# Optimization experiments

Measured on AMD Instinct MI355X. Metric: run time of the kernel, lower is better.

The kernel has to match this reference:

```python
import jax, jax.numpy as jnp
import numpy as np

B, Cin, Cout, H, W, K, S, P = 8, 128, 128, 64, 64, 3, 1, 1


def setup_inputs() -> dict:
    key = jax.random.key(0)
    k1, k2, k3 = jax.random.split(key, 3)
    x = jax.random.normal(k1, (B, Cin, H, W), jnp.float32)
    # offset-predicting conv weight (zero-init in the original; use small random for a nontrivial test)
    w_offset = jax.random.normal(k2, (2 * K * K, Cin, K, K), jnp.float32) * 0.01
    # deformable conv weight, uniform(-stdv, stdv) with stdv = 1/sqrt(Cin*K*K)
    stdv = 1.0 / np.sqrt(Cin * K * K)
    w = jax.random.uniform(k3, (Cout, Cin, K, K), jnp.float32, -stdv, stdv)
    return {"x": x, "w_offset": w_offset, "w": w}


def _conv2d(x, w, stride, pad):
    return jax.lax.conv_general_dilated(
        x, w, (stride, stride), [(pad, pad), (pad, pad)],
        dimension_numbers=("NCHW", "OIHW", "NCHW"))


def _deform_conv(x, offset, w, stride, pad):
    # x: [B,C,H,W]; offset: [B,2*K*K,Ho,Wo] as (dy,dx) pairs per kernel tap; w: [Cout,C,K,K]
    Bb, C, Hh, Ww = x.shape
    Co, _, Kk, _ = w.shape
    _, _, Ho, Wo = offset.shape
    KK = Kk * Kk
    off = offset.reshape(Bb, KK, 2, Ho, Wo)
    dy, dx = off[:, :, 0], off[:, :, 1]              # [B,KK,Ho,Wo]

    ky, kx = jnp.meshgrid(jnp.arange(Kk), jnp.arange(Kk), indexing="ij")
    ky = ky.reshape(KK).astype(x.dtype)
    kx = kx.reshape(KK).astype(x.dtype)
    oy = (jnp.arange(Ho) * stride - pad).astype(x.dtype)
    ox = (jnp.arange(Wo) * stride - pad).astype(x.dtype)

    # absolute sampling coordinates per kernel tap: [B,KK,Ho,Wo]
    py = oy[None, None, :, None] + ky[None, :, None, None] + dy
    px = ox[None, None, None, :] + kx[None, :, None, None] + dx

    y0 = jnp.floor(py)
    x0 = jnp.floor(px)
    ly = py - y0
    lx = px - x0
    y0i = y0.astype(jnp.int32)
    x0i = x0.astype(jnp.int32)

    xf = x.reshape(Bb, C, Hh * Ww)

    def gather(yi, xi):
        valid = (yi >= 0) & (yi < Hh) & (xi >= 0) & (xi < Ww)
        yc = jnp.clip(yi, 0, Hh - 1)
        xc = jnp.clip(xi, 0, Ww - 1)
        idx = (yc * Ww + xc).reshape(Bb, -1)          # [B, KK*Ho*Wo]
        v = jax.vmap(lambda xb, ib: xb[:, ib])(xf, idx)  # [B, C, KK*Ho*Wo]
        return v * valid.reshape(Bb, 1, -1).astype(x.dtype)

    v00 = gather(y0i, x0i)
    v01 = gather(y0i, x0i + 1)
    v10 = gather(y0i + 1, x0i)
    v11 = gather(y0i + 1, x0i + 1)

    wy = ly.reshape(Bb, 1, -1)
    wx = lx.reshape(Bb, 1, -1)
    sampled = (v00 * (1 - wy) * (1 - wx) + v01 * (1 - wy) * wx
               + v10 * wy * (1 - wx) + v11 * wy * wx)   # [B, C, KK*Ho*Wo]
    sampled = sampled.reshape(Bb, C, KK, Ho * Wo)

    out = jnp.einsum("bckl,ock->bol", sampled, w.reshape(Co, C, KK))
    return out.reshape(Bb, Co, Ho, Wo)


def reference(x, w_offset, w):
    offset = _conv2d(x, w_offset, S, P)   # [B, 2*K*K, Ho, Wo]
    return _deform_conv(x, offset, w, S, P)
```

## Files before the change

### kernel.cpp

```cpp
#include <hip/hip_runtime.h>
#include <hip/hip_bf16.h>
#include <math.h>


typedef short bf16x8 __attribute__((ext_vector_type(8)));
typedef float f32x4  __attribute__((ext_vector_type(4)));

__device__ __forceinline__ unsigned short f2bf(float f) {
    unsigned u = __float_as_uint(f);
    u += 0x7fffu + ((u >> 16) & 1u);
    return (unsigned short)(u >> 16);
}
__device__ __forceinline__ float bflo(unsigned u) { return __uint_as_float(u << 16); }
__device__ __forceinline__ float bfhi(unsigned u) { return __uint_as_float(u & 0xffff0000u); }

__global__ __launch_bounds__(256) void prep_weights(
    const float* __restrict__ w, const float* __restrict__ woff,
    unsigned short* __restrict__ wT, unsigned short* __restrict__ woffT) {
    int idx = blockIdx.x * 256 + threadIdx.x;
    if (idx < 147456) {
        int c  = idx & 127;
        int co = (idx >> 7) & 127;
        int kk = idx >> 14;
        wT[idx] = f2bf(w[co * 1152 + c * 9 + kk]);
    }
    if (idx < 36864) {
        int c  = idx & 127;
        int oc = (idx >> 7) & 31;
        int kk = idx >> 12;
        woffT[idx] = (oc < 18) ? f2bf(woff[oc * 1152 + c * 9 + kk]) : (unsigned short)0;
    }
}

__global__ __launch_bounds__(256) void transpose_nchw_nhwc(
    const float* __restrict__ x, unsigned* __restrict__ xT) {
    __shared__ float tile[128][65];
    int bh = blockIdx.x;
    int b = bh >> 6, h = bh & 63;
    const float* src = x + b * 524288 + h * 64;
    for (int idx = threadIdx.x; idx < 8192; idx += 256) {
        int c = idx >> 6, ww = idx & 63;
        tile[c][ww] = src[c * 4096 + ww];
    }
    __syncthreads();
    unsigned* dst = xT + (size_t)bh * 4096;
    for (int idx = threadIdx.x; idx < 4096; idx += 256) {
        int ww = idx >> 6, c2 = (idx & 63) * 2;
        unsigned lo = f2bf(tile[c2][ww]);
        unsigned hi = f2bf(tile[c2 + 1][ww]);
        dst[idx] = lo | (hi << 16);
    }
}

__global__ __launch_bounds__(512, 4) void deform_fused(
    const __hip_bfloat16* __restrict__ xT,
    const unsigned short* __restrict__ wT,
    const unsigned short* __restrict__ woffT,
    float* __restrict__ out) {
    __shared__ unsigned short s_tile[2][8192];
    __shared__ float  s_off[18][64];
    __shared__ int4   s_pix[576];
    __shared__ float4 s_wt[576];

    int raw = blockIdx.x;
    int b  = raw & 7;
    int ho = raw >> 3;
    int t = threadIdx.x, l = t & 63, w = t >> 6;
    int lr = l & 15, lg = l >> 4;
    const char* xb = (const char*)xT + (size_t)b * 1048576;

    {
        int m4 = w >> 1, n2 = w & 1;
        f32x4 oacc = {0.f, 0.f, 0.f, 0.f};
        for (int kk = 0; kk < 9; ++kk) {
            int y = ho + kk / 3 - 1;
            if ((unsigned)y >= 64u) continue;
            int xcol = m4 * 16 + lr + kk % 3 - 1;
            bool vx = (unsigned)xcol < 64u;
            const unsigned short* wo = woffT + (kk * 32 + n2 * 16 + lr) * 128 + lg * 8;
#pragma unroll
            for (int kg = 0; kg < 4; ++kg) {
                bf16x8 A = {};
                if (vx) A = *(const bf16x8*)(xb + ((y * 64 + xcol) * 128 + kg * 32 + lg * 8) * 2);
                bf16x8 Bf = *(const bf16x8*)(wo + kg * 32);
                oacc = __builtin_amdgcn_mfma_f32_16x16x32_bf16(A, Bf, oacc, 0, 0, 0);
            }
        }
        int oc = n2 * 16 + lr;
        if (oc < 18) {
#pragma unroll
            for (int r = 0; r < 4; ++r)
                s_off[oc][m4 * 16 + lg * 4 + r] = oacc[r];
        }
    }
    __syncthreads();

    for (int e = t; e < 576; e += 512) {
        int pos = e & 63, kk = e >> 6;
        float dy = s_off[2 * kk][pos], dx = s_off[2 * kk + 1][pos];
        float py = (float)(ho + kk / 3 - 1) + dy;
        float px = (float)(pos + kk % 3 - 1) + dx;
        float y0f = floorf(py), x0f = floorf(px);
        float ly = py - y0f, lx = px - x0f;
        int y0 = (int)y0f, x0 = (int)x0f;
        int y1 = y0 + 1, x1 = x0 + 1;
        float my0 = ((unsigned)y0 < 64u) ? 1.f : 0.f;
        float my1 = ((unsigned)y1 < 64u) ? 1.f : 0.f;
        float mx0 = ((unsigned)x0 < 64u) ? 1.f : 0.f;
        float mx1 = ((unsigned)x1 < 64u) ? 1.f : 0.f;
        int y0c = min(max(y0, 0), 63), y1c = min(max(y1, 0), 63);
        int x0c = min(max(x0, 0), 63), x1c = min(max(x1, 0), 63);
        s_pix[e] = make_int4((y0c * 64 + x0c) * 256, (y0c * 64 + x1c) * 256,
                             (y1c * 64 + x0c) * 256, (y1c * 64 + x1c) * 256);
        s_wt[e] = make_float4((1.f - ly) * (1.f - lx) * my0 * mx0,
                              (1.f - ly) * lx * my0 * mx1,
                              ly * (1.f - lx) * my1 * mx0,
                              ly * lx * my1 * mx1);
    }
    __syncthreads();

    int pg = t >> 5;
    int cq = t & 31;
    int cb = w * 16;
    int coff = cq * 8;
    f32x4 acc[4] = {{0.f,0.f,0.f,0.f},{0.f,0.f,0.f,0.f},{0.f,0.f,0.f,0.f},{0.f,0.f,0.f,0.f}};
    uint2 u[4][4];

    auto issue = [&](int kk) {
#pragma unroll
        for (int i = 0; i < 4; ++i) {
            int pos = pg + i * 16;
            int4 pix = s_pix[kk * 64 + pos];
            u[i][0] = *(const uint2*)(xb + pix.x + coff);
            u[i][1] = *(const uint2*)(xb + pix.y + coff);
            u[i][2] = *(const uint2*)(xb + pix.z + coff);
            u[i][3] = *(const uint2*)(xb + pix.w + coff);
        }
    };
    auto process = [&](int kk, int buf) {
        char* tp = (char*)s_tile[buf];
#pragma unroll
        for (int i = 0; i < 4; ++i) {
            int pos = pg + i * 16;
            float4 wt = s_wt[kk * 64 + pos];
            float r0 = wt.x * bflo(u[i][0].x) + wt.y * bflo(u[i][1].x) + wt.z * bflo(u[i][2].x) + wt.w * bflo(u[i][3].x);
            float r1 = wt.x * bfhi(u[i][0].x) + wt.y * bfhi(u[i][1].x) + wt.z * bfhi(u[i][2].x) + wt.w * bfhi(u[i][3].x);
            float r2 = wt.x * bflo(u[i][0].y) + wt.y * bflo(u[i][1].y) + wt.z * bflo(u[i][2].y) + wt.w * bflo(u[i][3].y);
            float r3 = wt.x * bfhi(u[i][0].y) + wt.y * bfhi(u[i][1].y) + wt.z * bfhi(u[i][2].y) + wt.w * bfhi(u[i][3].y);
            uint2 o;
            o.x = (unsigned)f2bf(r0) | ((unsigned)f2bf(r1) << 16);
            o.y = (unsigned)f2bf(r2) | ((unsigned)f2bf(r3) << 16);
            *(uint2*)(tp + pos * 256 + (((cq >> 1) ^ (pos & 7)) << 4) + (cq & 1) * 8) = o;
        }
    };

    issue(0);
    process(0, 0);
    __syncthreads();

    for (int kk = 0; kk < 9; ++kk) {
        if (kk < 8) issue(kk + 1);
        __builtin_amdgcn_sched_barrier(0);
        {
            const unsigned short* wr = wT + ((kk * 128 + cb + lr) << 7) + lg * 8;
            bf16x8 Af[4];
#pragma unroll
            for (int kg = 0; kg < 4; ++kg)
                Af[kg] = *(const bf16x8*)(wr + kg * 32);
            char* rp = (char*)s_tile[kk & 1];
#pragma unroll
            for (int kg = 0; kg < 4; ++kg) {
                int slot = kg * 4 + lg;
#pragma unroll
                for (int n = 0; n < 4; ++n) {
                    int row = n * 16 + lr;
                    bf16x8 Bf = *(const bf16x8*)(rp + row * 256 + ((slot ^ (row & 7)) << 4));
                    acc[n] = __builtin_amdgcn_mfma_f32_16x16x32_bf16(Af[kg], Bf, acc[n], 0, 0, 0);
                }
            }
        }
        __builtin_amdgcn_sched_barrier(0);
        if (kk < 8) process(kk + 1, (kk + 1) & 1);
        __syncthreads();
    }

    float* ob = out + ((size_t)(b * 128 + cb + lg * 4)) * 4096 + ho * 64;
#pragma unroll
    for (int n = 0; n < 4; ++n) {
#pragma unroll
        for (int r = 0; r < 4; ++r)
            ob[r * 4096 + n * 16 + lr] = acc[n][r];
    }
}

extern "C" void kernel_launch(void* const* d_in, const int* in_sizes, int n_in,
                              void* d_out, int out_size, void* d_ws, size_t ws_size,
                              hipStream_t stream) {
    const float* x    = (const float*)d_in[0];
    const float* woff = (const float*)d_in[1];
    const float* w    = (const float*)d_in[2];
    float* out = (float*)d_out;

    unsigned short* wT    = (unsigned short*)d_ws;
    unsigned short* woffT = (unsigned short*)((char*)d_ws + 294912);
    __hip_bfloat16* xT    = (__hip_bfloat16*)((char*)d_ws + 368640);

    prep_weights<<<576, 256, 0, stream>>>(w, woff, wT, woffT);
    transpose_nchw_nhwc<<<512, 256, 0, stream>>>(x, (unsigned*)xT);
    deform_fused<<<512, 512, 0, stream>>>(xT, wT, woffT, out);
}
```

Before: 146.2 us.

## Switch to fp16 and build MFMA operands in registers, dropping the LDS sample tile

```diff
diff --git a/kernel.cpp b/kernel.cpp
--- a/kernel.cpp
+++ b/kernel.cpp
@@ -3,32 +3,27 @@
 #include <math.h>
 
 
-typedef short bf16x8 __attribute__((ext_vector_type(8)));
-typedef float f32x4  __attribute__((ext_vector_type(4)));
+typedef _Float16 f16x8 __attribute__((ext_vector_type(8)));
+typedef _Float16 h2    __attribute__((ext_vector_type(2)));
+typedef float    f32x4 __attribute__((ext_vector_type(4)));
 
-__device__ __forceinline__ unsigned short f2bf(float f) {
-    unsigned u = __float_as_uint(f);
-    u += 0x7fffu + ((u >> 16) & 1u);
-    return (unsigned short)(u >> 16);
-}
-__device__ __forceinline__ float bflo(unsigned u) { return __uint_as_float(u << 16); }
-__device__ __forceinline__ float bfhi(unsigned u) { return __uint_as_float(u & 0xffff0000u); }
+union U4 { uint4 u; h2 h[4]; f16x8 v; };
 
 __global__ __launch_bounds__(256) void prep_weights(
     const float* __restrict__ w, const float* __restrict__ woff,
-    unsigned short* __restrict__ wT, unsigned short* __restrict__ woffT) {
+    _Float16* __restrict__ wT, _Float16* __restrict__ woffT) {
     int idx = blockIdx.x * 256 + threadIdx.x;
     if (idx < 147456) {
         int c  = idx & 127;
         int co = (idx >> 7) & 127;
         int kk = idx >> 14;
-        wT[idx] = f2bf(w[co * 1152 + c * 9 + kk]);
+        wT[idx] = (_Float16)w[co * 1152 + c * 9 + kk];
     }
     if (idx < 36864) {
         int c  = idx & 127;
         int oc = (idx >> 7) & 31;
         int kk = idx >> 12;
-        woffT[idx] = (oc < 18) ? f2bf(woff[oc * 1152 + c * 9 + kk]) : (unsigned short)0;
+        woffT[idx] = (oc < 18) ? (_Float16)woff[oc * 1152 + c * 9 + kk] : (_Float16)0.f;
     }
 }
 
@@ -46,18 +41,17 @@
     unsigned* dst = xT + (size_t)bh * 4096;
     for (int idx = threadIdx.x; idx < 4096; idx += 256) {
         int ww = idx >> 6, c2 = (idx & 63) * 2;
-        unsigned lo = f2bf(tile[c2][ww]);
-        unsigned hi = f2bf(tile[c2 + 1][ww]);
-        dst[idx] = lo | (hi << 16);
+        union { h2 h; unsigned u; } p;
+        p.h = h2{(_Float16)tile[c2][ww], (_Float16)tile[c2 + 1][ww]};
+        dst[idx] = p.u;
     }
 }
 
-__global__ __launch_bounds__(512, 4) void deform_fused(
-    const __hip_bfloat16* __restrict__ xT,
-    const unsigned short* __restrict__ wT,
-    const unsigned short* __restrict__ woffT,
+__global__ __launch_bounds__(256, 2) void deform_fused(
+    const _Float16* __restrict__ xT,
+    const _Float16* __restrict__ wT,
+    const _Float16* __restrict__ woffT,
     float* __restrict__ out) {
-    __shared__ unsigned short s_tile[2][8192];
     __shared__ float  s_off[18][64];
     __shared__ int4   s_pix[576];
     __shared__ float4 s_wt[576];
@@ -70,32 +64,33 @@
     const char* xb = (const char*)xT + (size_t)b * 1048576;
 
     {
-        int m4 = w >> 1, n2 = w & 1;
-        f32x4 oacc = {0.f, 0.f, 0.f, 0.f};
+        f32x4 oacc0 = {0.f,0.f,0.f,0.f}, oacc1 = {0.f,0.f,0.f,0.f};
         for (int kk = 0; kk < 9; ++kk) {
             int y = ho + kk / 3 - 1;
             if ((unsigned)y >= 64u) continue;
-            int xcol = m4 * 16 + lr + kk % 3 - 1;
+            int xcol = w * 16 + lr + kk % 3 - 1;
             bool vx = (unsigned)xcol < 64u;
-            const unsigned short* wo = woffT + (kk * 32 + n2 * 16 + lr) * 128 + lg * 8;
+            const _Float16* wo = woffT + (kk * 32 + lr) * 128 + lg * 8;
 #pragma unroll
             for (int kg = 0; kg < 4; ++kg) {
-                bf16x8 A = {};
-                if (vx) A = *(const bf16x8*)(xb + ((y * 64 + xcol) * 128 + kg * 32 + lg * 8) * 2);
-                bf16x8 Bf = *(const bf16x8*)(wo + kg * 32);
-                oacc = __builtin_amdgcn_mfma_f32_16x16x32_bf16(A, Bf, oacc, 0, 0, 0);
+                f16x8 A = {};
+                if (vx) A = *(const f16x8*)(xb + ((y * 64 + xcol) * 128 + kg * 32 + lg * 8) * 2);
+                oacc0 = __builtin_amdgcn_mfma_f32_16x16x32_f16(A, *(const f16x8*)(wo + kg * 32),        oacc0, 0, 0, 0);
+                oacc1 = __builtin_amdgcn_mfma_f32_16x16x32_f16(A, *(const f16x8*)(wo + 2048 + kg * 32), oacc1, 0, 0, 0);
             }
         }
-        int oc = n2 * 16 + lr;
-        if (oc < 18) {
+#pragma unroll
+        for (int r = 0; r < 4; ++r)
+            s_off[lr][w * 16 + lg * 4 + r] = oacc0[r];
+        if (lr < 2) {
 #pragma unroll
             for (int r = 0; r < 4; ++r)
-                s_off[oc][m4 * 16 + lg * 4 + r] = oacc[r];
+                s_off[16 + lr][w * 16 + lg * 4 + r] = oacc1[r];
         }
     }
     __syncthreads();
 
-    for (int e = t; e < 576; e += 512) {
+    for (int e = t; e < 576; e += 256) {
         int pos = e & 63, kk = e >> 6;
         float dy = s_off[2 * kk][pos], dx = s_off[2 * kk + 1][pos];
         float py = (float)(ho + kk / 3 - 1) + dy;
@@ -119,78 +114,48 @@
     }
     __syncthreads();
 
-    int pg = t >> 5;
-    int cq = t & 31;
-    int cb = w * 16;
-    int coff = cq * 8;
-    f32x4 acc[4] = {{0.f,0.f,0.f,0.f},{0.f,0.f,0.f,0.f},{0.f,0.f,0.f,0.f},{0.f,0.f,0.f,0.f}};
-    uint2 u[4][4];
-
-    auto issue = [&](int kk) {
-#pragma unroll
-        for (int i = 0; i < 4; ++i) {
-            int pos = pg + i * 16;
-            int4 pix = s_pix[kk * 64 + pos];
-            u[i][0] = *(const uint2*)(xb + pix.x + coff);
-            u[i][1] = *(const uint2*)(xb + pix.y + coff);
-            u[i][2] = *(const uint2*)(xb + pix.z + coff);
-            u[i][3] = *(const uint2*)(xb + pix.w + coff);
-        }
-    };
-    auto process = [&](int kk, int buf) {
-        char* tp = (char*)s_tile[buf];
-#pragma unroll
-        for (int i = 0; i < 4; ++i) {
-            int pos = pg + i * 16;
-            float4 wt = s_wt[kk * 64 + pos];
-            float r0 = wt.x * bflo(u[i][0].x) + wt.y * bflo(u[i][1].x) + wt.z * bflo(u[i][2].x) + wt.w * bflo(u[i][3].x);
-            float r1 = wt.x * bfhi(u[i][0].x) + wt.y * bfhi(u[i][1].x) + wt.z * bfhi(u[i][2].x) + wt.w * bfhi(u[i][3].x);
-            float r2 = wt.x * bflo(u[i][0].y) + wt.y * bflo(u[i][1].y) + wt.z * bflo(u[i][2].y) + wt.w * bflo(u[i][3].y);
-            float r3 = wt.x * bfhi(u[i][0].y) + wt.y * bfhi(u[i][1].y) + wt.z * bfhi(u[i][2].y) + wt.w * bfhi(u[i][3].y);
-            uint2 o;
-            o.x = (unsigned)f2bf(r0) | ((unsigned)f2bf(r1) << 16);
-            o.y = (unsigned)f2bf(r2) | ((unsigned)f2bf(r3) << 16);
-            *(uint2*)(tp + pos * 256 + (((cq >> 1) ^ (pos & 7)) << 4) + (cq & 1) * 8) = o;
-        }
-    };
-
-    issue(0);
-    process(0, 0);
-    __syncthreads();
+    int wb = w * 16;
+    f32x4 acc[8] = {{0.f,0.f,0.f,0.f},{0.f,0.f,0.f,0.f},{0.f,0.f,0.f,0.f},{0.f,0.f,0.f,0.f},
+                    {0.f,0.f,0.f,0.f},{0.f,0.f,0.f,0.f},{0.f,0.f,0.f,0.f},{0.f,0.f,0.f,0.f}};
 
     for (int kk = 0; kk < 9; ++kk) {
-        if (kk < 8) issue(kk + 1);
-        __builtin_amdgcn_sched_barrier(0);
-        {
-            const unsigned short* wr = wT + ((kk * 128 + cb + lr) << 7) + lg * 8;
-            bf16x8 Af[4];
+        int e = kk * 64 + wb + lr;
+        int4 pix = s_pix[e];
+        float4 wt = s_wt[e];
+        _Float16 wx = (_Float16)wt.x, wy = (_Float16)wt.y,
+                 wz = (_Float16)wt.z, ww2 = (_Float16)wt.w;
+        h2 w0 = h2{wx, wx}, w1 = h2{wy, wy}, w2 = h2{wz, wz}, w3 = h2{ww2, ww2};
+
+        f16x8 a[4];
 #pragma unroll
-            for (int kg = 0; kg < 4; ++kg)
-                Af[kg] = *(const bf16x8*)(wr + kg * 32);
-            char* rp = (char*)s_tile[kk & 1];
+        for (int ks = 0; ks < 4; ++ks) {
+            int c2 = (ks * 32 + lg * 8) * 2;
+            U4 v00, v01, v10, v11, s;
+            v00.u = *(const uint4*)(xb + pix.x + c2);
+            v01.u = *(const uint4*)(xb + pix.y + c2);
+            v10.u = *(const uint4*)(xb + pix.z + c2);
+            v11.u = *(const uint4*)(xb + pix.w + c2);
 #pragma unroll
-            for (int kg = 0; kg < 4; ++kg) {
-                int slot = kg * 4 + lg;
+            for (int j = 0; j < 4; ++j)
+                s.h[j] = w0 * v00.h[j] + w1 * v01.h[j] + w2 * v10.h[j] + w3 * v11.h[j];
+            a[ks] = s.v;
+        }
+        const _Float16* wkk = wT + (kk * 128 + lr) * 128 + lg * 8;
 #pragma unroll
-                for (int n = 0; n < 4; ++n) {
-                    int row = n * 16 + lr;
-                    bf16x8 Bf = *(const bf16x8*)(rp + row * 256 + ((slot ^ (row & 7)) << 4));
-                    acc[n] = __builtin_amdgcn_mfma_f32_16x16x32_bf16(Af[kg], Bf, acc[n], 0, 0, 0);
-                }
+        for (int ks = 0; ks < 4; ++ks) {
+#pragma unroll
+            for (int cot = 0; cot < 8; ++cot) {
+                f16x8 Bf = *(const f16x8*)(wkk + cot * 2048 + ks * 32);
+                acc[cot] = __builtin_amdgcn_mfma_f32_16x16x32_f16(a[ks], Bf, acc[cot], 0, 0, 0);
             }
         }
-        __builtin_amdgcn_sched_barrier(0);
-        if (kk < 8) process(kk + 1, (kk + 1) & 1);
-        __syncthreads();
     }
 
-    float* ob = out + ((size_t)(b * 128 + cb + lg * 4)) * 4096 + ho * 64;
+    float* ob = out + ((size_t)(b * 128 + lr)) * 4096 + ho * 64 + wb + lg * 4;
 #pragma unroll
-    for (int n = 0; n < 4; ++n) {
-#pragma unroll
-        for (int r = 0; r < 4; ++r)
-            ob[r * 4096 + n * 16 + lr] = acc[n][r];
-    }
+    for (int cot = 0; cot < 8; ++cot)
+        *(float4*)(ob + (size_t)cot * 16 * 4096) =
+            make_float4(acc[cot][0], acc[cot][1], acc[cot][2], acc[cot][3]);
 }
 
 extern "C" void kernel_launch(void* const* d_in, const int* in_sizes, int n_in,
@@ -201,11 +166,11 @@
     const float* w    = (const float*)d_in[2];
     float* out = (float*)d_out;
 
-    unsigned short* wT    = (unsigned short*)d_ws;
-    unsigned short* woffT = (unsigned short*)((char*)d_ws + 294912);
-    __hip_bfloat16* xT    = (__hip_bfloat16*)((char*)d_ws + 368640);
+    _Float16* wT    = (_Float16*)d_ws;
+    _Float16* woffT = (_Float16*)((char*)d_ws + 294912);
+    _Float16* xT    = (_Float16*)((char*)d_ws + 368640);
 
     prep_weights<<<576, 256, 0, stream>>>(w, woff, wT, woffT);
     transpose_nchw_nhwc<<<512, 256, 0, stream>>>(x, (unsigned*)xT);
-    deform_fused<<<512, 512, 0, stream>>>(xT, wT, woffT, out);
+    deform_fused<<<512, 256, 0, stream>>>(xT, wT, woffT, out);
 }
```

Measured after the change: 194.1 us. 32.8% more time.

## Switch to fp16 with packed-half bilinear blend and prefetched weight fragments

Applied to the files above, without the earlier changes.

```diff
diff --git a/kernel.cpp b/kernel.cpp
--- a/kernel.cpp
+++ b/kernel.cpp
@@ -3,32 +3,25 @@
 #include <math.h>
 
 
-typedef short bf16x8 __attribute__((ext_vector_type(8)));
-typedef float f32x4  __attribute__((ext_vector_type(4)));
-
-__device__ __forceinline__ unsigned short f2bf(float f) {
-    unsigned u = __float_as_uint(f);
-    u += 0x7fffu + ((u >> 16) & 1u);
-    return (unsigned short)(u >> 16);
-}
-__device__ __forceinline__ float bflo(unsigned u) { return __uint_as_float(u << 16); }
-__device__ __forceinline__ float bfhi(unsigned u) { return __uint_as_float(u & 0xffff0000u); }
+typedef _Float16 f16x8 __attribute__((ext_vector_type(8)));
+typedef _Float16 h2    __attribute__((ext_vector_type(2)));
+typedef float    f32x4 __attribute__((ext_vector_type(4)));
 
 __global__ __launch_bounds__(256) void prep_weights(
     const float* __restrict__ w, const float* __restrict__ woff,
-    unsigned short* __restrict__ wT, unsigned short* __restrict__ woffT) {
+    _Float16* __restrict__ wT, _Float16* __restrict__ woffT) {
     int idx = blockIdx.x * 256 + threadIdx.x;
     if (idx < 147456) {
         int c  = idx & 127;
         int co = (idx >> 7) & 127;
         int kk = idx >> 14;
-        wT[idx] = f2bf(w[co * 1152 + c * 9 + kk]);
+        wT[idx] = (_Float16)w[co * 1152 + c * 9 + kk];
     }
     if (idx < 36864) {
         int c  = idx & 127;
         int oc = (idx >> 7) & 31;
         int kk = idx >> 12;
-        woffT[idx] = (oc < 18) ? f2bf(woff[oc * 1152 + c * 9 + kk]) : (unsigned short)0;
+        woffT[idx] = (oc < 18) ? (_Float16)woff[oc * 1152 + c * 9 + kk] : (_Float16)0.f;
     }
 }
 
@@ -46,16 +39,16 @@
     unsigned* dst = xT + (size_t)bh * 4096;
     for (int idx = threadIdx.x; idx < 4096; idx += 256) {
         int ww = idx >> 6, c2 = (idx & 63) * 2;
-        unsigned lo = f2bf(tile[c2][ww]);
-        unsigned hi = f2bf(tile[c2 + 1][ww]);
-        dst[idx] = lo | (hi << 16);
+        union { h2 h; unsigned u; } p;
+        p.h = h2{(_Float16)tile[c2][ww], (_Float16)tile[c2 + 1][ww]};
+        dst[idx] = p.u;
     }
 }
 
 __global__ __launch_bounds__(512, 4) void deform_fused(
-    const __hip_bfloat16* __restrict__ xT,
-    const unsigned short* __restrict__ wT,
-    const unsigned short* __restrict__ woffT,
+    const _Float16* __restrict__ xT,
+    const _Float16* __restrict__ wT,
+    const _Float16* __restrict__ woffT,
     float* __restrict__ out) {
     __shared__ unsigned short s_tile[2][8192];
     __shared__ float  s_off[18][64];
@@ -71,20 +64,28 @@
 
     {
         int m4 = w >> 1, n2 = w & 1;
+        f16x8 A[2][4];
         f32x4 oacc = {0.f, 0.f, 0.f, 0.f};
+        auto loadA = [&](int kk, f16x8* dst) {
+            int y = ho + kk / 3 - 1;
+            int xcol = m4 * 16 + lr + kk % 3 - 1;
+            bool valid = ((unsigned)y < 64u) && ((unsigned)xcol < 64u);
+            int yc = min(max(y, 0), 63), xc = min(max(xcol, 0), 63);
+            const char* p = xb + ((yc * 64 + xc) * 128 + lg * 8) * 2;
+            _Float16 m = (_Float16)(valid ? 1.f : 0.f);
+#pragma unroll
+            for (int kg = 0; kg < 4; ++kg)
+                dst[kg] = *(const f16x8*)(p + kg * 64) * m;
+        };
+        loadA(0, A[0]);
+#pragma unroll
         for (int kk = 0; kk < 9; ++kk) {
-            int y = ho + kk / 3 - 1;
-            if ((unsigned)y >= 64u) continue;
-            int xcol = m4 * 16 + lr + kk % 3 - 1;
-            bool vx = (unsigned)xcol < 64u;
-            const unsigned short* wo = woffT + (kk * 32 + n2 * 16 + lr) * 128 + lg * 8;
-#pragma unroll
-            for (int kg = 0; kg < 4; ++kg) {
-                bf16x8 A = {};
-                if (vx) A = *(const bf16x8*)(xb + ((y * 64 + xcol) * 128 + kg * 32 + lg * 8) * 2);
-                bf16x8 Bf = *(const bf16x8*)(wo + kg * 32);
-                oacc = __builtin_amdgcn_mfma_f32_16x16x32_bf16(A, Bf, oacc, 0, 0, 0);
-            }
+            if (kk < 8) loadA(kk + 1, A[(kk + 1) & 1]);
+            const _Float16* wo = woffT + (kk * 32 + n2 * 16 + lr) * 128 + lg * 8;
+#pragma unroll
+            for (int kg = 0; kg < 4; ++kg)
+                oacc = __builtin_amdgcn_mfma_f32_16x16x32_f16(
+                    A[kk & 1][kg], *(const f16x8*)(wo + kg * 32), oacc, 0, 0, 0);
         }
         int oc = n2 * 16 + lr;
         if (oc < 18) {
@@ -124,9 +125,16 @@
     int cb = w * 16;
     int coff = cq * 8;
     f32x4 acc[4] = {{0.f,0.f,0.f,0.f},{0.f,0.f,0.f,0.f},{0.f,0.f,0.f,0.f},{0.f,0.f,0.f,0.f}};
+    f16x8 W[2][4];
     uint2 u[4][4];
 
-    auto issue = [&](int kk) {
+    auto issueW = [&](int kk, f16x8* Wd) {
+        const _Float16* wr = wT + (kk * 128 + cb + lr) * 128 + lg * 8;
+#pragma unroll
+        for (int kg = 0; kg < 4; ++kg)
+            Wd[kg] = *(const f16x8*)(wr + kg * 32);
+    };
+    auto issueG = [&](int kk) {
 #pragma unroll
         for (int i = 0; i < 4; ++i) {
             int pos = pg + i * 16;
@@ -137,36 +145,37 @@
             u[i][3] = *(const uint2*)(xb + pix.w + coff);
         }
     };
-    auto process = [&](int kk, int buf) {
+    auto processW = [&](int kk, int buf) {
         char* tp = (char*)s_tile[buf];
 #pragma unroll
         for (int i = 0; i < 4; ++i) {
             int pos = pg + i * 16;
             float4 wt = s_wt[kk * 64 + pos];
-            float r0 = wt.x * bflo(u[i][0].x) + wt.y * bflo(u[i][1].x) + wt.z * bflo(u[i][2].x) + wt.w * bflo(u[i][3].x);
-            float r1 = wt.x * bfhi(u[i][0].x) + wt.y * bfhi(u[i][1].x) + wt.z * bfhi(u[i][2].x) + wt.w * bfhi(u[i][3].x);
-            float r2 = wt.x * bflo(u[i][0].y) + wt.y * bflo(u[i][1].y) + wt.z * bflo(u[i][2].y) + wt.w * bflo(u[i][3].y);
-            float r3 = wt.x * bfhi(u[i][0].y) + wt.y * bfhi(u[i][1].y) + wt.z * bfhi(u[i][2].y) + wt.w * bfhi(u[i][3].y);
-            uint2 o;
-            o.x = (unsigned)f2bf(r0) | ((unsigned)f2bf(r1) << 16);
-            o.y = (unsigned)f2bf(r2) | ((unsigned)f2bf(r3) << 16);
-            *(uint2*)(tp + pos * 256 + (((cq >> 1) ^ (pos & 7)) << 4) + (cq & 1) * 8) = o;
+            h2 w0 = h2{(_Float16)wt.x, (_Float16)wt.x};
+            h2 w1 = h2{(_Float16)wt.y, (_Float16)wt.y};
+            h2 w2 = h2{(_Float16)wt.z, (_Float16)wt.z};
+            h2 w3 = h2{(_Float16)wt.w, (_Float16)wt.w};
+            union { uint2 u2; h2 h[2]; } a0, a1, a2, a3, r;
+            a0.u2 = u[i][0]; a1.u2 = u[i][1]; a2.u2 = u[i][2]; a3.u2 = u[i][3];
+            r.h[0] = w0 * a0.h[0] + w1 * a1.h[0] + w2 * a2.h[0] + w3 * a3.h[0];
+            r.h[1] = w0 * a0.h[1] + w1 * a1.h[1] + w2 * a2.h[1] + w3 * a3.h[1];
+            *(uint2*)(tp + pos * 256 + (((cq >> 1) ^ (pos & 7)) << 4) + (cq & 1) * 8) = r.u2;
         }
     };
 
-    issue(0);
-    process(0, 0);
-    __syncthreads();
-
+    issueW(0, W[0]);
+    issueG(0);
+    processW(0, 0);
+    __syncthreads();
+
+#pragma unroll
     for (int kk = 0; kk < 9; ++kk) {
-        if (kk < 8) issue(kk + 1);
+        if (kk < 8) {
+            issueW(kk + 1, W[(kk + 1) & 1]);
+            issueG(kk + 1);
+        }
         __builtin_amdgcn_sched_barrier(0);
         {
-            const unsigned short* wr = wT + ((kk * 128 + cb + lr) << 7) + lg * 8;
-            bf16x8 Af[4];
-#pragma unroll
-            for (int kg = 0; kg < 4; ++kg)
-                Af[kg] = *(const bf16x8*)(wr + kg * 32);
             char* rp = (char*)s_tile[kk & 1];
 #pragma unroll
             for (int kg = 0; kg < 4; ++kg) {
@@ -174,13 +183,13 @@
 #pragma unroll
                 for (int n = 0; n < 4; ++n) {
                     int row = n * 16 + lr;
-                    bf16x8 Bf = *(const bf16x8*)(rp + row * 256 + ((slot ^ (row & 7)) << 4));
-                    acc[n] = __builtin_amdgcn_mfma_f32_16x16x32_bf16(Af[kg], Bf, acc[n], 0, 0, 0);
+                    f16x8 Bf = *(const f16x8*)(rp + row * 256 + ((slot ^ (row & 7)) << 4));
+                    acc[n] = __builtin_amdgcn_mfma_f32_16x16x32_f16(W[kk & 1][kg], Bf, acc[n], 0, 0, 0);
                 }
             }
         }
         __builtin_amdgcn_sched_barrier(0);
-        if (kk < 8) process(kk + 1, (kk + 1) & 1);
+        if (kk < 8) processW(kk + 1, (kk + 1) & 1);
         __syncthreads();
     }
 
@@ -201,9 +210,9 @@
     const float* w    = (const float*)d_in[2];
     float* out = (float*)d_out;
 
-    unsigned short* wT    = (unsigned short*)d_ws;
-    unsigned short* woffT = (unsigned short*)((char*)d_ws + 294912);
-    __hip_bfloat16* xT    = (__hip_bfloat16*)((char*)d_ws + 368640);
+    _Float16* wT    = (_Float16*)d_ws;
+    _Float16* woffT = (_Float16*)((char*)d_ws + 294912);
+    _Float16* xT    = (_Float16*)((char*)d_ws + 368640);
 
     prep_weights<<<576, 256, 0, stream>>>(w, woff, wT, woffT);
     transpose_nchw_nhwc<<<512, 256, 0, stream>>>(x, (unsigned*)xT);
```

New measurement: 144.5 us. Within noise of the previous version (-1.2%).
